# Optimization experiments

Measured on AMD Instinct MI355X. Metric: run time of the kernel, lower is better.

The kernel has to match this reference:

```python
import jax, jax.numpy as jnp
import numpy as np

INF = jnp.float32(1e9)


def _hungarian_min_perm(Cp, n):
    """Shortest-augmenting-path Hungarian (e-maxx variant) on padded cost Cp.
    Cp: (n+1, n+1) with Cp[i, j] = C[i-1, j-1] for i,j >= 1; row/col 0 virtual.
    Returns p: (n+1,) int32 where p[j] (j>=1) is the 1-based row assigned to col j.
    """
    cols = jnp.arange(n + 1)

    def outer(i, carry):
        u, v, p = carry
        p = p.at[0].set(i)
        init = (jnp.int32(0), u, v, p,
                jnp.full(n + 1, INF, Cp.dtype),
                jnp.zeros(n + 1, bool),
                jnp.zeros(n + 1, jnp.int32))

        def cond(s):
            j0, u, v, p, minv, used, way = s
            return p[j0] != 0

        def body(s):
            j0, u, v, p, minv, used, way = s
            used = used.at[j0].set(True)
            i0 = p[j0]
            cur = Cp[i0] - u[i0] - v                      # reduced costs, (n+1,)
            avail = (~used) & (cols >= 1)
            better = avail & (cur < minv)
            minv = jnp.where(better, cur, minv)
            way = jnp.where(better, j0, way)
            mv = jnp.where(avail, minv, INF)
            j1 = jnp.argmin(mv).astype(jnp.int32)
            delta = mv[j1]
            u = u.at[p].add(jnp.where(used, delta, 0.0))  # u[p[j]] += delta for used j
            v = v - jnp.where(used, delta, 0.0)
            minv = jnp.where(used, minv, minv - delta)
            return (j1, u, v, p, minv, used, way)

        j0, u, v, p, minv, used, way = jax.lax.while_loop(cond, body, init)

        # reconstruct augmenting path
        def cond2(s):
            return s[0] != 0

        def body2(s):
            j0, p = s
            j1 = way[j0]
            return (j1, p.at[j0].set(p[j1]))

        _, p = jax.lax.while_loop(cond2, body2, (j0, p))
        return (u, v, p)

    u0 = jnp.zeros(n + 1, Cp.dtype)
    v0 = jnp.zeros(n + 1, Cp.dtype)
    p0 = jnp.zeros(n + 1, jnp.int32)
    _, _, p = jax.lax.fori_loop(1, n + 1, outer, (u0, v0, p0))
    return p


def hungarian_maximize(a):
    """a: (n, n) benefit matrix -> (n, n) 0/1 optimal assignment matrix (maximize)."""
    n = a.shape[0]
    Cp = jnp.zeros((n + 1, n + 1), a.dtype).at[1:, 1:].set(-a)  # minimize -a
    p = _hungarian_min_perm(Cp, n)
    return jnp.zeros((n, n), jnp.float32).at[p[1:] - 1, jnp.arange(n)].set(1.0)


batched_lsa = jax.vmap(hungarian_maximize)


def setup_inputs() -> dict:
    key = jax.random.key(0)
    B, H, W = 1024, 128, 128
    x = jax.random.normal(key, (B, H, W), dtype=jnp.float32)
    bias = jnp.ones((H, W), dtype=jnp.float32)  # nn.Parameter(torch.ones(h, w))
    return {"x": x, "bias": bias}


def reference(x, bias):
    perm = batched_lsa(x)                               # (B, h, w) 0/1 assignments
    out = perm / jnp.sqrt(jnp.sum(perm * perm))         # global L2 norm (dim=None, keepdim)
    out = out * bias                                    # broadcast (h, w)
    return jax.nn.softmax(out, axis=2)                  # w >= h -> softmax over dim 2
```

## Files before the change

kernel.cpp:

```cpp
#include <hip/hip_runtime.h>
#include <hip/hip_fp16.h>

#define N 128
#define INF_ 1e9f
typedef unsigned long long ull;

__device__ __forceinline__ unsigned f2ord(float f) {
    unsigned b = __float_as_uint(f);
    return b ^ ((unsigned)((int)b >> 31) | 0x80000000u);
}
__device__ __forceinline__ float ord2f(unsigned k) {
    unsigned b = k ^ ((unsigned)((int)(~k) >> 31) | 0x80000000u);
    return __uint_as_float(b);
}
template <int CTRL>
__device__ __forceinline__ int dppmov(int v) {
    return __builtin_amdgcn_update_dpp(v, v, CTRL, 0xF, 0xF, false);
}
__device__ __forceinline__ int rl(int v, int lane) { return __builtin_amdgcn_readlane(v, lane); }
__device__ __forceinline__ unsigned rlu(unsigned v, int lane) {
    return (unsigned)__builtin_amdgcn_readlane((int)v, lane);
}
__device__ __forceinline__ unsigned uminu(unsigned a, unsigned b) { return a < b ? a : b; }

#define GMIN16(k) { \
    k = uminu(k, (unsigned)dppmov<0x121>((int)k)); \
    k = uminu(k, (unsigned)dppmov<0x122>((int)k)); \
    k = uminu(k, (unsigned)dppmov<0x124>((int)k)); \
    k = uminu(k, (unsigned)dppmov<0x128>((int)k)); \
}
#define GMINALL(k, gmin) { \
    unsigned _g0 = rlu(k, 0), _g1 = rlu(k, 16), _g2 = rlu(k, 32), _g3 = rlu(k, 48); \
    gmin = uminu(uminu(_g0, _g1), uminu(_g2, _g3)); \
}

__global__ void __launch_bounds__(64) lsa_solve_kernel(
        const float* __restrict__ x, const float* __restrict__ bias,
        float* __restrict__ out, int B) {
    __shared__ unsigned Cs[N][64];
    __shared__ float u_lds[N + 1];
    __shared__ int   colOf[N + 1];
    __shared__ int   freeQ[N + 1];

    const int b = blockIdx.x;
    const int l = threadIdx.x;
    const int c0 = 2 * l + 1, c1 = 2 * l + 2;
    const ull mlt = (1ull << l) - 1;
    const float* xb = x + (size_t)b * (N * N);

    #pragma unroll 4
    for (int r = 0; r < N; ++r) {
        const float2 f = *(const float2*)&xb[r * N + 2 * l];
        __half2 h = __floats2half2_rn(-f.x, -f.y);
        Cs[r][l] = __builtin_bit_cast(unsigned, h);
    }
    u_lds[l] = 0.f;   u_lds[l + 64] = 0.f;
    colOf[l + 1] = 0; colOf[l + 65] = 0;
    freeQ[l] = 0x7FFFFFFF; freeQ[l + 64] = 0x7FFFFFFF;
    if (l == 0) { u_lds[128] = 0.f; colOf[0] = 0; freeQ[128] = 0x7FFFFFFF; }
    __syncthreads();

    float m0 = INF_, m1 = INF_; int am0 = 1, am1 = 1;
    #pragma unroll 4
    for (int r = 0; r < N; ++r) {
        __half2 h = __builtin_bit_cast(__half2, Cs[r][l]);
        float f0 = __low2float(h), f1 = __high2float(h);
        if (f0 < m0) { m0 = f0; am0 = r + 1; }
        if (f1 < m1) { m1 = f1; am1 = r + 1; }
    }
    float v0r = m0, v1r = m1;
    atomicMin(&freeQ[am0], c0);
    atomicMin(&freeQ[am1], c1);
    __syncthreads();
    int prow0 = (freeQ[am0] == c0) ? am0 : 0;
    int prow1 = (freeQ[am1] == c1) ? am1 : 0;
    if (prow0) colOf[am0] = c0;
    if (prow1) colOf[am1] = c1;
    __syncthreads();

    {
        float pend0 = 0.f, pend1 = 0.f;
        #pragma unroll 2
        for (int r = 1; r <= N; ++r) {
            int j1 = __builtin_amdgcn_readfirstlane(colOf[r]);
            __half2 h = __builtin_bit_cast(__half2, Cs[r - 1][l]);
            float rc0 = __low2float(h)  - v0r;
            float rc1 = __high2float(h) - v1r;
            if (c0 == j1) rc0 = INF_;
            if (c1 == j1) rc1 = INF_;
            unsigned k = uminu(f2ord(rc0), f2ord(rc1));
            GMIN16(k)
            unsigned gmin; GMINALL(k, gmin)
            float m2 = ord2f(gmin);
            if (j1 != 0) {
                if (c0 == j1) pend0 = m2;
                if (c1 == j1) pend1 = m2;
            }
        }
        v0r -= pend0; v1r -= pend1;
    }

    int nf;
    {
        int fA = (colOf[l + 1] == 0);
        int fB = (colOf[l + 65] == 0);
        ull bA = __ballot(fA), bB = __ballot(fB);
        int nA = __popcll(bA);
        if (fA) freeQ[__popcll(bA & mlt)] = l + 1;
        if (fB) freeQ[nA + __popcll(bB & mlt)] = l + 65;
        nf = nA + __popcll(bB);
    }
    __syncthreads();

    {
        int prv = nf;
        #pragma unroll 1
        for (int pass = 0; pass < 2 && prv > 0; ++pass) {
            int wr = 0;
            #pragma unroll 1
            for (int kk = 0; kk < prv; ++kk) {
                const int i = __builtin_amdgcn_readfirstlane(freeQ[kk]);
                __half2 h = __builtin_bit_cast(__half2, Cs[i - 1][l]);
                float rc0 = __low2float(h)  - v0r;
                float rc1 = __high2float(h) - v1r;
                unsigned k0 = f2ord(rc0), k1 = f2ord(rc1);
                unsigned klmin = uminu(k0, k1);
                int isHi = (k1 < k0) ? 1 : 0;
                unsigned kg = klmin;
                GMIN16(kg)
                unsigned gmin; GMINALL(kg, gmin)
                ull bw = __ballot(klmin == gmin);
                int wl = (int)__builtin_ctzll(bw);
                int hi1 = rl(isHi, wl);
                int j1 = 2 * wl + 1 + hi1;
                unsigned oth = (l == wl) ? (hi1 ? k0 : k1) : klmin;
                unsigned kg2 = oth;
                GMIN16(kg2)
                unsigned m2o; GMINALL(kg2, m2o)
                if (gmin < m2o) {
                    float d = ord2f(m2o) - ord2f(gmin);
                    if (c0 == j1) v0r -= d;
                    if (c1 == j1) v1r -= d;
                } else {
                    int sl1 = (j1 - 1) >> 1;
                    int pj1 = ((j1 - 1) & 1) ? rl(prow1, sl1) : rl(prow0, sl1);
                    if (pj1 != 0) {
                        ull bw2 = __ballot(oth == m2o);
                        int wl2 = (int)__builtin_ctzll(bw2);
                        int hi2 = (wl2 == wl) ? (hi1 ^ 1) : rl(isHi, wl2);
                        j1 = 2 * wl2 + 1 + hi2;
                    }
                }
                int slj = (j1 - 1) >> 1;
                int inc = ((j1 - 1) & 1) ? rl(prow1, slj) : rl(prow0, slj);
                if (c0 == j1) prow0 = i;
                if (c1 == j1) prow1 = i;
                if (l == 0) {
                    colOf[i] = j1;
                    if (inc != 0) { colOf[inc] = 0; freeQ[wr] = inc; }
                }
                if (inc != 0) ++wr;
            }
            prv = wr;
            __syncthreads();
        }
    }

    {
        int fA = (colOf[l + 1] == 0);
        int fB = (colOf[l + 65] == 0);
        ull bA = __ballot(fA), bB = __ballot(fB);
        int nA = __popcll(bA);
        if (fA) freeQ[__popcll(bA & mlt)] = l + 1;
        if (fB) freeQ[nA + __popcll(bB & mlt)] = l + 65;
        nf = nA + __popcll(bB);
    }
    __syncthreads();
    int qv0 = freeQ[l], qv1 = freeQ[l + 64];

    #pragma unroll 1
    for (int fi = 0; fi < nf; ++fi) {
        int sl = fi & 63;
        const int i = (fi < 64) ? rl(qv0, sl) : rl(qv1, sl);
        __half2 h = __builtin_bit_cast(__half2, Cs[i - 1][l]);
        float rc0 = __low2float(h)  - v0r;
        float rc1 = __high2float(h) - v1r;
        unsigned k0 = f2ord(rc0), k1 = f2ord(rc1);
        unsigned kl = uminu(k0, k1);
        int isHi = (k1 < k0) ? 1 : 0;
        unsigned kg = kl;
        GMIN16(kg)
        unsigned gmin; GMINALL(kg, gmin)
        ull bw = __ballot(kl == gmin);
        int wl = (int)__builtin_ctzll(bw);
        int hi = rl(isHi, wl);
        int jm = 2 * wl + 1 + hi;
        if (l == 0) u_lds[i] = ord2f(gmin);
        int slm = (jm - 1) >> 1;
        int pm = ((jm - 1) & 1) ? rl(prow1, slm) : rl(prow0, slm);
        if (pm == 0) {
            if (c0 == jm) prow0 = i;
            if (c1 == jm) prow1 = i;
            if (l == 0) colOf[i] = jm;
        }
    }
    __syncthreads();

    if (prow0) {
        __half2 h = __builtin_bit_cast(__half2, Cs[prow0 - 1][l]);
        u_lds[prow0] = __low2float(h) - v0r;
    }
    if (prow1) {
        __half2 h = __builtin_bit_cast(__half2, Cs[prow1 - 1][l]);
        u_lds[prow1] = __high2float(h) - v1r;
    }
    __syncthreads();

    {
        int fA = (colOf[l + 1] == 0);
        int fB = (colOf[l + 65] == 0);
        ull bA = __ballot(fA), bB = __ballot(fB);
        int nA = __popcll(bA);
        if (fA) freeQ[__popcll(bA & mlt)] = l + 1;
        if (fB) freeQ[nA + __popcll(bB & mlt)] = l + 65;
        nf = nA + __popcll(bB);
    }
    __syncthreads();
    qv0 = freeQ[l]; qv1 = freeQ[l + 64];
    float uprow0 = u_lds[prow0], uprow1 = u_lds[prow1];

    #pragma unroll 1
    for (int fi = 0; fi < nf; ++fi) {
        int sl = fi & 63;
        const int i = (fi < 64) ? rl(qv0, sl) : rl(qv1, sl);

        float dist0 = INF_, dist1 = INF_;
        int   way0 = 0, way1 = 0;
        float cumAt0 = 0.f, cumAt1 = 0.f;
        float cum = 0.f;
        float base = -u_lds[i];
        int   j0 = 0, i0 = i;

        #pragma unroll 1
        for (int it = 0; it <= N; ++it) {
            if (c0 == j0) { cumAt0 = cum; dist0 = __int_as_float(0x7FC00000); }
            if (c1 == j0) { cumAt1 = cum; dist1 = __int_as_float(0x7FC00000); }

            __half2 h = __builtin_bit_cast(__half2, Cs[i0 - 1][l]);
            float cand0 = __low2float(h)  - v0r + base;
            float cand1 = __high2float(h) - v1r + base;
            if (cand0 < dist0) { dist0 = cand0; way0 = j0; }
            if (cand1 < dist1) { dist1 = cand1; way1 = j0; }

            unsigned k0 = f2ord(dist0), k1 = f2ord(dist1);
            unsigned kl = uminu(k0, k1);
            int isHi = (k1 < k0) ? 1 : 0;
            unsigned kg = kl;
            GMIN16(kg)
            unsigned gmin; GMINALL(kg, gmin)
            ull bw = __ballot(kl == gmin);
            int wl = (int)__builtin_ctzll(bw);
            int hi = rl(isHi, wl);
            int pA = rl(prow0, wl), pB = rl(prow1, wl);
            int uA = rl(__float_as_int(uprow0), wl), uB = rl(__float_as_int(uprow1), wl);
            cum  = ord2f(gmin);
            j0   = 2 * wl + 1 + hi;
            i0   = hi ? pB : pA;
            base = cum - __int_as_float(hi ? uB : uA);
            if (i0 == 0) break;
        }

        bool used0 = (__float_as_uint(dist0) == 0x7FC00000u);
        bool used1 = (__float_as_uint(dist1) == 0x7FC00000u);
        if (used0) { float dv = cum - cumAt0; v0r -= dv; u_lds[prow0] += dv; }
        if (used1) { float dv = cum - cumAt1; v1r -= dv; u_lds[prow1] += dv; }
        if (l == 0) u_lds[i] += cum;
        __syncthreads();

        int j = j0;
        #pragma unroll 1
        while (j != 0) {
            int idx = j - 1, slw = idx >> 1, hib = idx & 1;
            int w0 = rl(way0, slw), w1 = rl(way1, slw);
            int jn = hib ? w1 : w0;
            int pn;
            if (jn == 0) pn = i;
            else {
                int pidx = jn - 1, slp = pidx >> 1, phb = pidx & 1;
                int p0 = rl(prow0, slp), p1 = rl(prow1, slp);
                pn = phb ? p1 : p0;
            }
            if (c0 == j) prow0 = pn;
            if (c1 == j) prow1 = pn;
            j = jn;
        }
        uprow0 = u_lds[prow0];
        uprow1 = u_lds[prow1];
    }

    colOf[prow0] = c0;
    colOf[prow1] = c1;
    __syncthreads();

    const float inv_norm = rsqrtf((float)B * (float)N);
    float* ob = out + (size_t)b * (N * N);
    #pragma unroll 2
    for (int r = 0; r < N; ++r) {
        int jA = __builtin_amdgcn_readfirstlane(colOf[r + 1]);
        float s = bias[r * N + (jA - 1)] * inv_norm;
        float e = __expf(s);
        float inv_d = 1.0f / (127.0f + e);
        float av = e * inv_d;
        float2 w;
        w.x = (c0 == jA) ? av : inv_d;
        w.y = (c1 == jA) ? av : inv_d;
        *(float2*)&ob[r * N + 2 * l] = w;
    }
}

extern "C" void kernel_launch(void* const* d_in, const int* in_sizes, int n_in,
                              void* d_out, int out_size, void* d_ws, size_t ws_size,
                              hipStream_t stream) {
    const float* x    = (const float*)d_in[0];
    const float* bias = (const float*)d_in[1];
    float* out = (float*)d_out;
    int B = in_sizes[0] / (N * N);
    hipLaunchKernelGGL(lsa_solve_kernel, dim3(B), dim3(64), 0, stream, x, bias, out, B);
}
```

Before: 308.8 us.

## Cache per-row reduced-cost minima to overlap Dijkstra step with row min

Replaces the two-pass auction-style augmenting-row-reduction with a per-row chained displacement loop bounded by a budget. Adds a precomputed per-row minimum of reduced cost (with argmin and cost) that the Dijkstra loop reuses to choose the next column. When the cached argmin is still unused and valid, it skips recomputing the row reduction, and the old-dist reduction can proceed independently of the new row's. The cost is a full extra row-min sweep over all 128 rows, extra readlanes, a fallback path, and more register pressure.

After: 609.7 us. +97.5%, slower.

```diff
diff --git a/kernel.cpp b/kernel.cpp
--- a/kernel.cpp
+++ b/kernel.cpp
@@ -3,6 +3,7 @@
 
 #define N 128
 #define INF_ 1e9f
+#define QNAN_U 0x7FC00000u
 typedef unsigned long long ull;
 
 __device__ __forceinline__ unsigned f2ord(float f) {
@@ -20,6 +21,9 @@
 __device__ __forceinline__ int rl(int v, int lane) { return __builtin_amdgcn_readlane(v, lane); }
 __device__ __forceinline__ unsigned rlu(unsigned v, int lane) {
     return (unsigned)__builtin_amdgcn_readlane((int)v, lane);
+}
+__device__ __forceinline__ float rlf(float v, int lane) {
+    return __int_as_float(__builtin_amdgcn_readlane(__float_as_int(v), lane));
 }
 __device__ __forceinline__ unsigned uminu(unsigned a, unsigned b) { return a < b ? a : b; }
 
@@ -32,6 +36,16 @@
 #define GMINALL(k, gmin) { \
     unsigned _g0 = rlu(k, 0), _g1 = rlu(k, 16), _g2 = rlu(k, 32), _g3 = rlu(k, 48); \
     gmin = uminu(uminu(_g0, _g1), uminu(_g2, _g3)); \
+}
+#define RLPAIR_I(r0, r1, idx, dst) { \
+    int _ln = ((idx) - 1) >> 1; \
+    int _a = rl(r0, _ln), _b = rl(r1, _ln); \
+    dst = (((idx) - 1) & 1) ? _b : _a; \
+}
+#define RLPAIR_F(r0, r1, idx, dst) { \
+    int _ln = ((idx) - 1) >> 1; \
+    float _a = rlf(r0, _ln), _b = rlf(r1, _ln); \
+    dst = (((idx) - 1) & 1) ? _b : _a; \
 }
 
 __global__ void __launch_bounds__(64) lsa_solve_kernel(
@@ -113,27 +127,28 @@
     __syncthreads();
 
     {
-        int prv = nf;
+        int budget = 3 * nf + 16;
+        bool stop = false;
         #pragma unroll 1
-        for (int pass = 0; pass < 2 && prv > 0; ++pass) {
-            int wr = 0;
+        for (int kk = 0; kk < nf && !stop; ++kk) {
+            int i = __builtin_amdgcn_readfirstlane(freeQ[kk]);
             #pragma unroll 1
-            for (int kk = 0; kk < prv; ++kk) {
-                const int i = __builtin_amdgcn_readfirstlane(freeQ[kk]);
+            while (i != 0) {
+                if (--budget < 0) { stop = true; break; }
                 __half2 h = __builtin_bit_cast(__half2, Cs[i - 1][l]);
                 float rc0 = __low2float(h)  - v0r;
                 float rc1 = __high2float(h) - v1r;
                 unsigned k0 = f2ord(rc0), k1 = f2ord(rc1);
-                unsigned klmin = uminu(k0, k1);
+                unsigned klm = uminu(k0, k1);
                 int isHi = (k1 < k0) ? 1 : 0;
-                unsigned kg = klmin;
+                unsigned kg = klm;
                 GMIN16(kg)
                 unsigned gmin; GMINALL(kg, gmin)
-                ull bw = __ballot(klmin == gmin);
+                ull bw = __ballot(klm == gmin);
                 int wl = (int)__builtin_ctzll(bw);
                 int hi1 = rl(isHi, wl);
                 int j1 = 2 * wl + 1 + hi1;
-                unsigned oth = (l == wl) ? (hi1 ? k0 : k1) : klmin;
+                unsigned oth = (l == wl) ? (hi1 ? k0 : k1) : klm;
                 unsigned kg2 = oth;
                 GMIN16(kg2)
                 unsigned m2o; GMINALL(kg2, m2o)
@@ -142,8 +157,7 @@
                     if (c0 == j1) v0r -= d;
                     if (c1 == j1) v1r -= d;
                 } else {
-                    int sl1 = (j1 - 1) >> 1;
-                    int pj1 = ((j1 - 1) & 1) ? rl(prow1, sl1) : rl(prow0, sl1);
+                    int pj1; RLPAIR_I(prow0, prow1, j1, pj1)
                     if (pj1 != 0) {
                         ull bw2 = __ballot(oth == m2o);
                         int wl2 = (int)__builtin_ctzll(bw2);
@@ -151,19 +165,17 @@
                         j1 = 2 * wl2 + 1 + hi2;
                     }
                 }
-                int slj = (j1 - 1) >> 1;
-                int inc = ((j1 - 1) & 1) ? rl(prow1, slj) : rl(prow0, slj);
+                int disp; RLPAIR_I(prow0, prow1, j1, disp)
                 if (c0 == j1) prow0 = i;
                 if (c1 == j1) prow1 = i;
                 if (l == 0) {
                     colOf[i] = j1;
-                    if (inc != 0) { colOf[inc] = 0; freeQ[wr] = inc; }
+                    if (disp != 0) colOf[disp] = 0;
                 }
-                if (inc != 0) ++wr;
-            }
-            prv = wr;
-            __syncthreads();
-        }
+                i = disp;
+            }
+        }
+        __syncthreads();
     }
 
     {
@@ -196,8 +208,7 @@
         int hi = rl(isHi, wl);
         int jm = 2 * wl + 1 + hi;
         if (l == 0) u_lds[i] = ord2f(gmin);
-        int slm = (jm - 1) >> 1;
-        int pm = ((jm - 1) & 1) ? rl(prow1, slm) : rl(prow0, slm);
+        int pm; RLPAIR_I(prow0, prow1, jm, pm)
         if (pm == 0) {
             if (c0 == jm) prow0 = i;
             if (c1 == jm) prow1 = i;
@@ -215,6 +226,33 @@
         u_lds[prow1] = __high2float(h) - v1r;
     }
     __syncthreads();
+
+    float cm0 = 0.f, cm1 = 0.f; int mt0 = 0, mt1 = 0;
+    #pragma unroll 2
+    for (int r = 1; r <= N; ++r) {
+        unsigned roww = Cs[r - 1][l];
+        __half2 h = __builtin_bit_cast(__half2, roww);
+        float rc0 = __low2float(h)  - v0r;
+        float rc1 = __high2float(h) - v1r;
+        unsigned q0 = f2ord(rc0), q1 = f2ord(rc1);
+        unsigned ql = uminu(q0, q1);
+        int qHi = (q1 < q0) ? 1 : 0;
+        unsigned qg = ql;
+        GMIN16(qg)
+        unsigned g; GMINALL(qg, g)
+        ull bw = __ballot(ql == g);
+        int wl = (int)__builtin_ctzll(bw);
+        int hi = rl(qHi, wl);
+        int arg = 2 * wl + 1 + hi;
+        unsigned ww = rlu(roww, wl);
+        int c16 = hi ? (int)(ww >> 16) : (int)(ww & 0xFFFF);
+        float m = ord2f(g);
+        int cl2 = (r - 1) >> 1;
+        if (l == cl2) {
+            if ((r - 1) & 1) { cm1 = m; mt1 = (c16 << 8) | arg; }
+            else             { cm0 = m; mt0 = (c16 << 8) | arg; }
+        }
+    }
 
     {
         int fA = (colOf[l + 1] == 0);
@@ -239,45 +277,107 @@
         float cumAt0 = 0.f, cumAt1 = 0.f;
         float cum = 0.f;
         float base = -u_lds[i];
-        int   j0 = 0, i0 = i;
+        int   jcur = 0, i0 = i;
+        ull usedLo = 0, usedHi = 0;
 
         #pragma unroll 1
         for (int it = 0; it <= N; ++it) {
-            if (c0 == j0) { cumAt0 = cum; dist0 = __int_as_float(0x7FC00000); }
-            if (c1 == j0) { cumAt1 = cum; dist1 = __int_as_float(0x7FC00000); }
-
-            __half2 h = __builtin_bit_cast(__half2, Cs[i0 - 1][l]);
-            float cand0 = __low2float(h)  - v0r + base;
-            float cand1 = __high2float(h) - v1r + base;
-            if (cand0 < dist0) { dist0 = cand0; way0 = j0; }
-            if (cand1 < dist1) { dist1 = cand1; way1 = j0; }
+            if (c0 == jcur) { cumAt0 = cum; dist0 = __int_as_float(QNAN_U); }
+            if (c1 == jcur) { cumAt1 = cum; dist1 = __int_as_float(QNAN_U); }
+            if (jcur != 0) {
+                if (jcur <= 64) usedLo |= 1ull << (jcur - 1);
+                else            usedHi |= 1ull << (jcur - 65);
+            }
+
+            unsigned roww = Cs[i0 - 1][l];
+
+            int cl2 = (i0 - 1) >> 1;
+            bool ohalf = (i0 - 1) & 1;
+            float cmA = rlf(cm0, cl2), cmB = rlf(cm1, cl2);
+            int   mtA = rl(mt0, cl2),  mtB = rl(mt1, cl2);
+            float mC = ohalf ? cmB : cmA;
+            int   mt = ohalf ? mtB : mtA;
+            int argC = mt & 0xFF;
+            unsigned c16 = ((unsigned)mt >> 8) & 0xFFFFu;
+            float ccost = __low2float(__builtin_bit_cast(__half2, c16));
+            float vnow; RLPAIR_F(v0r, v1r, argC, vnow)
+            bool argUsed = (argC <= 64) ? ((usedLo >> (argC - 1)) & 1)
+                                        : ((usedHi >> (argC - 65)) & 1);
+            bool cvalid = (!argUsed) && ((ccost - vnow) == mC);
 
             unsigned k0 = f2ord(dist0), k1 = f2ord(dist1);
             unsigned kl = uminu(k0, k1);
             int isHi = (k1 < k0) ? 1 : 0;
+            int  pay  = isHi ? ((1 << 8) | prow1) : prow0;
+            float upay = isHi ? uprow1 : uprow0;
             unsigned kg = kl;
             GMIN16(kg)
-            unsigned gmin; GMINALL(kg, gmin)
-            ull bw = __ballot(kl == gmin);
-            int wl = (int)__builtin_ctzll(bw);
-            int hi = rl(isHi, wl);
-            int pA = rl(prow0, wl), pB = rl(prow1, wl);
-            int uA = rl(__float_as_int(uprow0), wl), uB = rl(__float_as_int(uprow1), wl);
-            cum  = ord2f(gmin);
-            j0   = 2 * wl + 1 + hi;
-            i0   = hi ? pB : pA;
-            base = cum - __int_as_float(hi ? uB : uA);
+            unsigned gA; GMINALL(kg, gA)
+            ull bwA = __ballot(kl == gA);
+            int wlA = (int)__builtin_ctzll(bwA);
+            int payA = rl(pay, wlA);
+            float uA = rlf(upay, wlA);
+            int jA = 2 * wlA + 1 + ((payA >> 8) & 1);
+            int iA = payA & 0xFF;
+
+            float mB; int jB;
+            if (cvalid) {
+                mB = mC; jB = argC;
+            } else {
+                __half2 h = __builtin_bit_cast(__half2, roww);
+                float rc0 = __low2float(h)  - v0r;
+                float rc1 = __high2float(h) - v1r;
+                if (__float_as_uint(dist0) == QNAN_U) rc0 = __int_as_float(QNAN_U);
+                if (__float_as_uint(dist1) == QNAN_U) rc1 = __int_as_float(QNAN_U);
+                unsigned q0 = f2ord(rc0), q1 = f2ord(rc1);
+                unsigned ql = uminu(q0, q1);
+                int qHi = (q1 < q0) ? 1 : 0;
+                unsigned qg = ql;
+                GMIN16(qg)
+                unsigned gB; GMINALL(qg, gB)
+                ull bwB = __ballot(ql == gB);
+                int wlB = (int)__builtin_ctzll(bwB);
+                int hiB = rl(qHi, wlB);
+                jB = 2 * wlB + 1 + hiB;
+                mB = ord2f(gB);
+                unsigned ww = rlu(roww, wlB);
+                int cc = hiB ? (int)(ww >> 16) : (int)(ww & 0xFFFF);
+                if (l == cl2) {
+                    if (ohalf) { cm1 = mB; mt1 = (cc << 8) | jB; }
+                    else       { cm0 = mB; mt0 = (cc << 8) | jB; }
+                }
+            }
+            unsigned kB = f2ord(mB + base);
+
+            bool bwin = (kB < gA) || (kB == gA && jB < jA);
+            float cum_new = ord2f(bwin ? kB : gA);
+            int jwin = bwin ? jB : jA;
+            int inext; float unext;
+            if (bwin) {
+                RLPAIR_I(prow0, prow1, jB, inext)
+                RLPAIR_F(uprow0, uprow1, jB, unext)
+            } else { inext = iA; unext = uA; }
+
+            {
+                __half2 h = __builtin_bit_cast(__half2, roww);
+                float cand0 = __low2float(h)  - v0r + base;
+                float cand1 = __high2float(h) - v1r + base;
+                if (cand0 < dist0) { dist0 = cand0; way0 = jcur; }
+                if (cand1 < dist1) { dist1 = cand1; way1 = jcur; }
+            }
+
+            cum = cum_new; jcur = jwin; i0 = inext; base = cum - unext;
             if (i0 == 0) break;
         }
 
-        bool used0 = (__float_as_uint(dist0) == 0x7FC00000u);
-        bool used1 = (__float_as_uint(dist1) == 0x7FC00000u);
+        bool used0 = (__float_as_uint(dist0) == QNAN_U);
+        bool used1 = (__float_as_uint(dist1) == QNAN_U);
         if (used0) { float dv = cum - cumAt0; v0r -= dv; u_lds[prow0] += dv; }
         if (used1) { float dv = cum - cumAt1; v1r -= dv; u_lds[prow1] += dv; }
         if (l == 0) u_lds[i] += cum;
         __syncthreads();
 
-        int j = j0;
+        int j = jcur;
         #pragma unroll 1
         while (j != 0) {
             int idx = j - 1, slw = idx >> 1, hib = idx & 1;
```

## Speculatively prefetch candidate cost rows per 16-lane group in Dijkstra loop

Applied to the files above, without the earlier changes.

In the augmenting-path inner loop, each 16-lane group's local minimum winner is found before the cross-group reduction. The row index and dual value it carries are read for all four groups, and their cost rows are loaded from LDS speculatively. The final winner then picks one of the four prefetched rows, which takes the LDS load off the serial dependency chain of the next iteration at the cost of extra readlanes and four loads per step. The diff also raises the auction-style preassignment from two passes to three and folds repeated readlane-pair code into a macro.

Result: slower. 372.2 us (+20.6%).

```diff
diff --git a/kernel.cpp b/kernel.cpp
--- a/kernel.cpp
+++ b/kernel.cpp
@@ -3,6 +3,7 @@
 
 #define N 128
 #define INF_ 1e9f
+#define QNAN_U 0x7FC00000u
 typedef unsigned long long ull;
 
 __device__ __forceinline__ unsigned f2ord(float f) {
@@ -20,6 +21,9 @@
 __device__ __forceinline__ int rl(int v, int lane) { return __builtin_amdgcn_readlane(v, lane); }
 __device__ __forceinline__ unsigned rlu(unsigned v, int lane) {
     return (unsigned)__builtin_amdgcn_readlane((int)v, lane);
+}
+__device__ __forceinline__ float rlf(float v, int lane) {
+    return __int_as_float(__builtin_amdgcn_readlane(__float_as_int(v), lane));
 }
 __device__ __forceinline__ unsigned uminu(unsigned a, unsigned b) { return a < b ? a : b; }
 
@@ -32,6 +36,11 @@
 #define GMINALL(k, gmin) { \
     unsigned _g0 = rlu(k, 0), _g1 = rlu(k, 16), _g2 = rlu(k, 32), _g3 = rlu(k, 48); \
     gmin = uminu(uminu(_g0, _g1), uminu(_g2, _g3)); \
+}
+#define RLPAIR_I(r0, r1, idx, dst) { \
+    int _ln = ((idx) - 1) >> 1; \
+    int _a = rl(r0, _ln), _b = rl(r1, _ln); \
+    dst = (((idx) - 1) & 1) ? _b : _a; \
 }
 
 __global__ void __launch_bounds__(64) lsa_solve_kernel(
@@ -115,7 +124,7 @@
     {
         int prv = nf;
         #pragma unroll 1
-        for (int pass = 0; pass < 2 && prv > 0; ++pass) {
+        for (int pass = 0; pass < 3 && prv > 0; ++pass) {
             int wr = 0;
             #pragma unroll 1
             for (int kk = 0; kk < prv; ++kk) {
@@ -124,16 +133,16 @@
                 float rc0 = __low2float(h)  - v0r;
                 float rc1 = __high2float(h) - v1r;
                 unsigned k0 = f2ord(rc0), k1 = f2ord(rc1);
-                unsigned klmin = uminu(k0, k1);
+                unsigned klm = uminu(k0, k1);
                 int isHi = (k1 < k0) ? 1 : 0;
-                unsigned kg = klmin;
+                unsigned kg = klm;
                 GMIN16(kg)
                 unsigned gmin; GMINALL(kg, gmin)
-                ull bw = __ballot(klmin == gmin);
+                ull bw = __ballot(klm == gmin);
                 int wl = (int)__builtin_ctzll(bw);
                 int hi1 = rl(isHi, wl);
                 int j1 = 2 * wl + 1 + hi1;
-                unsigned oth = (l == wl) ? (hi1 ? k0 : k1) : klmin;
+                unsigned oth = (l == wl) ? (hi1 ? k0 : k1) : klm;
                 unsigned kg2 = oth;
                 GMIN16(kg2)
                 unsigned m2o; GMINALL(kg2, m2o)
@@ -142,8 +151,7 @@
                     if (c0 == j1) v0r -= d;
                     if (c1 == j1) v1r -= d;
                 } else {
-                    int sl1 = (j1 - 1) >> 1;
-                    int pj1 = ((j1 - 1) & 1) ? rl(prow1, sl1) : rl(prow0, sl1);
+                    int pj1; RLPAIR_I(prow0, prow1, j1, pj1)
                     if (pj1 != 0) {
                         ull bw2 = __ballot(oth == m2o);
                         int wl2 = (int)__builtin_ctzll(bw2);
@@ -151,15 +159,14 @@
                         j1 = 2 * wl2 + 1 + hi2;
                     }
                 }
-                int slj = (j1 - 1) >> 1;
-                int inc = ((j1 - 1) & 1) ? rl(prow1, slj) : rl(prow0, slj);
+                int disp; RLPAIR_I(prow0, prow1, j1, disp)
                 if (c0 == j1) prow0 = i;
                 if (c1 == j1) prow1 = i;
                 if (l == 0) {
                     colOf[i] = j1;
-                    if (inc != 0) { colOf[inc] = 0; freeQ[wr] = inc; }
+                    if (disp != 0) { colOf[disp] = 0; freeQ[wr] = disp; }
                 }
-                if (inc != 0) ++wr;
+                if (disp != 0) ++wr;
             }
             prv = wr;
             __syncthreads();
@@ -196,8 +203,7 @@
         int hi = rl(isHi, wl);
         int jm = 2 * wl + 1 + hi;
         if (l == 0) u_lds[i] = ord2f(gmin);
-        int slm = (jm - 1) >> 1;
-        int pm = ((jm - 1) & 1) ? rl(prow1, slm) : rl(prow0, slm);
+        int pm; RLPAIR_I(prow0, prow1, jm, pm)
         if (pm == 0) {
             if (c0 == jm) prow0 = i;
             if (c1 == jm) prow1 = i;
@@ -239,45 +245,66 @@
         float cumAt0 = 0.f, cumAt1 = 0.f;
         float cum = 0.f;
         float base = -u_lds[i];
-        int   j0 = 0, i0 = i;
+        int   jcur = 0, i0 = i;
+        unsigned roww = Cs[i - 1][l];
 
         #pragma unroll 1
         for (int it = 0; it <= N; ++it) {
-            if (c0 == j0) { cumAt0 = cum; dist0 = __int_as_float(0x7FC00000); }
-            if (c1 == j0) { cumAt1 = cum; dist1 = __int_as_float(0x7FC00000); }
-
-            __half2 h = __builtin_bit_cast(__half2, Cs[i0 - 1][l]);
+            if (c0 == jcur) { cumAt0 = cum; dist0 = __int_as_float(QNAN_U); }
+            if (c1 == jcur) { cumAt1 = cum; dist1 = __int_as_float(QNAN_U); }
+
+            __half2 h = __builtin_bit_cast(__half2, roww);
             float cand0 = __low2float(h)  - v0r + base;
             float cand1 = __high2float(h) - v1r + base;
-            if (cand0 < dist0) { dist0 = cand0; way0 = j0; }
-            if (cand1 < dist1) { dist1 = cand1; way1 = j0; }
+            if (cand0 < dist0) { dist0 = cand0; way0 = jcur; }
+            if (cand1 < dist1) { dist1 = cand1; way1 = jcur; }
 
             unsigned k0 = f2ord(dist0), k1 = f2ord(dist1);
             unsigned kl = uminu(k0, k1);
             int isHi = (k1 < k0) ? 1 : 0;
+            int   pay  = isHi ? ((1 << 8) | prow1) : prow0;
+            float upay = isHi ? uprow1 : uprow0;
+
             unsigned kg = kl;
             GMIN16(kg)
-            unsigned gmin; GMINALL(kg, gmin)
-            ull bw = __ballot(kl == gmin);
-            int wl = (int)__builtin_ctzll(bw);
-            int hi = rl(isHi, wl);
-            int pA = rl(prow0, wl), pB = rl(prow1, wl);
-            int uA = rl(__float_as_int(uprow0), wl), uB = rl(__float_as_int(uprow1), wl);
-            cum  = ord2f(gmin);
-            j0   = 2 * wl + 1 + hi;
-            i0   = hi ? pB : pA;
-            base = cum - __int_as_float(hi ? uB : uA);
+            ull bw = __ballot(kl == kg);
+            int wl0 = (int)__builtin_ctzll(bw & 0xFFFFull);
+            int wl1 = 16 + (int)__builtin_ctzll((bw >> 16) & 0xFFFFull);
+            int wl2 = 32 + (int)__builtin_ctzll((bw >> 32) & 0xFFFFull);
+            int wl3 = 48 + (int)__builtin_ctzll((bw >> 48) & 0xFFFFull);
+            unsigned g0 = rlu(kg, 0), g1 = rlu(kg, 16), g2 = rlu(kg, 32), g3 = rlu(kg, 48);
+            int pay0 = rl(pay, wl0), pay1 = rl(pay, wl1);
+            int pay2 = rl(pay, wl2), pay3 = rl(pay, wl3);
+            float up0 = rlf(upay, wl0), up1 = rlf(upay, wl1);
+            float up2 = rlf(upay, wl2), up3 = rlf(upay, wl3);
+            int r0i = pay0 & 0xFF, r1i = pay1 & 0xFF, r2i = pay2 & 0xFF, r3i = pay3 & 0xFF;
+            unsigned w0 = Cs[(r0i > 0 ? r0i : 1) - 1][l];
+            unsigned w1 = Cs[(r1i > 0 ? r1i : 1) - 1][l];
+            unsigned w2 = Cs[(r2i > 0 ? r2i : 1) - 1][l];
+            unsigned w3 = Cs[(r3i > 0 ? r3i : 1) - 1][l];
+            unsigned gb = g0; int bi = 0;
+            if (g1 < gb) { gb = g1; bi = 1; }
+            if (g2 < gb) { gb = g2; bi = 2; }
+            if (g3 < gb) { gb = g3; bi = 3; }
+            int payb  = (bi == 0) ? pay0 : (bi == 1) ? pay1 : (bi == 2) ? pay2 : pay3;
+            float ub  = (bi == 0) ? up0 : (bi == 1) ? up1 : (bi == 2) ? up2 : up3;
+            int wlb   = (bi == 0) ? wl0 : (bi == 1) ? wl1 : (bi == 2) ? wl2 : wl3;
+            cum  = ord2f(gb);
+            jcur = 2 * wlb + 1 + ((payb >> 8) & 1);
+            i0   = payb & 0xFF;
+            base = cum - ub;
             if (i0 == 0) break;
-        }
-
-        bool used0 = (__float_as_uint(dist0) == 0x7FC00000u);
-        bool used1 = (__float_as_uint(dist1) == 0x7FC00000u);
+            roww = (bi == 0) ? w0 : (bi == 1) ? w1 : (bi == 2) ? w2 : w3;
+        }
+
+        bool used0 = (__float_as_uint(dist0) == QNAN_U);
+        bool used1 = (__float_as_uint(dist1) == QNAN_U);
         if (used0) { float dv = cum - cumAt0; v0r -= dv; u_lds[prow0] += dv; }
         if (used1) { float dv = cum - cumAt1; v1r -= dv; u_lds[prow1] += dv; }
         if (l == 0) u_lds[i] += cum;
         __syncthreads();
 
-        int j = j0;
+        int j = jcur;
         #pragma unroll 1
         while (j != 0) {
             int idx = j - 1, slw = idx >> 1, hib = idx & 1;
```
